# Optimization experiments

Measured on AMD Instinct MI355X. Metric: run time of the kernel, lower is better.

Reference implementation:

```python
import jax, jax.numpy as jnp
import numpy as np
import math

B, S, D_MODEL, H, D_LATENT = 2, 2048, 2048, 16, 512
D_HEAD = D_MODEL // H


def setup_inputs() -> dict:
    key = jax.random.key(0)
    ks = jax.random.split(key, 6)
    s = lambda fan: 1.0 / math.sqrt(fan)
    return {
        "x": jax.random.normal(ks[0], (B, S, D_MODEL), dtype=jnp.float32),
        "W_q": jax.random.normal(ks[1], (D_MODEL, D_MODEL), dtype=jnp.float32) * s(D_MODEL),
        "W_down_kv": jax.random.normal(ks[2], (D_LATENT, D_MODEL), dtype=jnp.float32) * s(D_MODEL),
        "W_up_k": jax.random.normal(ks[3], (H, D_HEAD, D_LATENT), dtype=jnp.float32) * s(D_LATENT),
        "W_up_v": jax.random.normal(ks[4], (H, D_HEAD, D_LATENT), dtype=jnp.float32) * s(D_LATENT),
        "W_o": jax.random.normal(ks[5], (D_MODEL, D_MODEL), dtype=jnp.float32) * s(D_MODEL),
    }


def reference(x, W_q, W_down_kv, W_up_k, W_up_v, W_o):
    b, s_len, d_model = x.shape
    # Q: (B, H, S, Dh)
    Q = (x @ W_q.T).reshape(b, s_len, H, D_HEAD).transpose(0, 2, 1, 3)
    # latent KV: (B, S, d_latent)
    C_kv = x @ W_down_kv.T
    # per-head up-projections fused into one einsum: (B, H, S, Dh)
    K = jnp.einsum("bsl,hdl->bhsd", C_kv, W_up_k)
    V = jnp.einsum("bsl,hdl->bhsd", C_kv, W_up_v)
    scores = jnp.einsum("bhsd,bhtd->bhst", Q, K) / math.sqrt(D_HEAD)
    attn = jax.nn.softmax(scores, axis=-1)  # dropout p=0 / eval -> identity
    out = jnp.einsum("bhst,bhtd->bhsd", attn, V)
    out = out.transpose(0, 2, 1, 3).reshape(b, s_len, H * D_HEAD)
    return out @ W_o.T
```

## Files before the change

kernel.cpp:

```cpp
#include <hip/hip_runtime.h>
#include <hip/hip_bf16.h>

typedef __hip_bfloat16 bf16;
typedef __attribute__((ext_vector_type(8))) short short8v;
typedef __attribute__((ext_vector_type(4))) short short4v;
typedef __attribute__((ext_vector_type(4))) float f32x4;
typedef __attribute__((ext_vector_type(16))) float f32x16;
typedef __attribute__((ext_vector_type(4))) unsigned int uint4v;
typedef unsigned int u32;

#define MFMA_16x16x32(a, b, c) __builtin_amdgcn_mfma_f32_16x16x32_bf16((a), (b), (c), 0, 0, 0)
#define MFMA_32x32x16(a, b, c) __builtin_amdgcn_mfma_f32_32x32x16_bf16((a), (b), (c), 0, 0, 0)

constexpr int Bc = 2, Sc = 2048, DMc = 2048, Hc = 16, DLc = 512, DHc = 128;

__device__ __forceinline__ void gload_lds16(const bf16* g, void* lds) {
  __builtin_amdgcn_global_load_lds(
      (const __attribute__((address_space(1))) void*)g,
      (__attribute__((address_space(3))) void*)lds, 16, 0, 0);
}

__device__ __forceinline__ unsigned short bf16bits(float f) {
  return __builtin_bit_cast(unsigned short, __float2bfloat16(f));
}

struct CvtArgs {
  const float* src[6];
  bf16* dst[6];
  unsigned int cum[6];
  unsigned int total4;
};

__global__ __launch_bounds__(256) void cvt_all_kernel(CvtArgs a)
{
  unsigned int i = blockIdx.x * 256 + threadIdx.x;
  const unsigned int stride = gridDim.x * 256;
  for (; i < a.total4; i += stride) {
    int s = 0;
#pragma unroll
    for (int k = 1; k < 6; ++k) s += (i >= a.cum[k]) ? 1 : 0;
    unsigned int off = (i - a.cum[s]) * 4;
    float4 v = *(const float4*)(a.src[s] + off);
    short4v p;
    p[0] = (short)bf16bits(v.x);
    p[1] = (short)bf16bits(v.y);
    p[2] = (short)bf16bits(v.z);
    p[3] = (short)bf16bits(v.w);
    *(short4v*)(a.dst[s] + off) = p;
  }
}

#define GPHASE(bufv, KK, MH)                                                \
  do {                                                                      \
    const char* ap_ = aR + (bufv) * 32768 + (KK) * 8192 + (MH) * 4096;      \
    const char* bp_ = bR + (bufv) * 32768 + (KK) * 8192;                    \
    short8v af_[4], bf_[4];                                                 \
    _Pragma("unroll")                                                       \
    for (int m4 = 0; m4 < 4; ++m4)                                          \
      af_[m4] = *(const short8v*)(ap_ + m4 * 1024);                         \
    _Pragma("unroll")                                                       \
    for (int n = 0; n < 4; ++n)                                             \
      bf_[n] = *(const short8v*)(bp_ + n * 1024);                           \
    __builtin_amdgcn_s_setprio(1);                                          \
    _Pragma("unroll")                                                       \
    for (int m4 = 0; m4 < 4; ++m4)                                          \
      _Pragma("unroll")                                                     \
      for (int n = 0; n < 4; ++n)                                           \
        acc[(MH) * 4 + m4][n] =                                             \
            MFMA_16x16x32(af_[m4], bf_[n], acc[(MH) * 4 + m4][n]);          \
    __builtin_amdgcn_s_setprio(0);                                          \
  } while (0)

template<int EPI>
__device__ __forceinline__ void gemm_tile_256(
    const bf16* __restrict__ A, const bf16* __restrict__ BT, void* __restrict__ Cv,
    int K, int ldc, int row0, int col0, char* AsC, char* BsC)
{
  const int tid = threadIdx.x;
  const int lane = tid & 63, wid = tid >> 6;
  const int wm = wid >> 2, wn = wid & 3;
  const int fr = lane & 15, g = lane >> 4;

  f32x4 acc[8][4] = {};

  const int srow = tid >> 2;
  const int scolS = ((tid & 3) * 16) ^ (((srow >> 1) & 3) << 4);
  const bf16* sA = A + (size_t)(row0 + srow) * K + (scolS >> 1);
  const bf16* sB = BT + (size_t)(col0 + srow) * K + (scolS >> 1);
  char* AsW = AsC + wid * 1024;
  char* BsW = BsC + wid * 1024;

  auto ISSA = [&](int buf, int h, int kk, int kt) {
    gload_lds16(sA + (size_t)(h * 128) * K + kt * 64 + kk * 32,
                AsW + buf * 32768 + h * 16384 + kk * 8192);
  };
  auto ISSB = [&](int buf, int h, int kk, int kt) {
    gload_lds16(sB + (size_t)(h * 128) * K + kt * 64 + kk * 32,
                BsW + buf * 32768 + h * 16384 + kk * 8192);
  };

  const int rdLane = fr * 64 + ((g * 16) ^ (((fr >> 1) & 3) << 4));
  const char* aR = AsC + wm * 16384 + rdLane;
  const char* bR = BsC + (wn >> 1) * 16384 + (wn & 1) * 4096 + rdLane;

  ISSA(0, 0, 0, 0); ISSA(0, 1, 0, 0); ISSB(0, 0, 0, 0); ISSB(0, 1, 0, 0);
  ISSA(0, 0, 1, 0); ISSA(0, 1, 1, 0); ISSB(0, 0, 1, 0); ISSB(0, 1, 1, 0);

  const int KT = K >> 6;
  for (int kt = 0; kt < KT - 1; ++kt) {
    const int buf = kt & 1, nb = buf ^ 1;
    asm volatile("s_waitcnt vmcnt(4)" ::: "memory");
    __builtin_amdgcn_s_barrier();
    asm volatile("" ::: "memory");
    ISSA(nb, 0, 0, kt + 1); ISSA(nb, 1, 0, kt + 1);
    GPHASE(buf, 0, 0);
    ISSB(nb, 0, 0, kt + 1); ISSB(nb, 1, 0, kt + 1);
    GPHASE(buf, 0, 1);
    asm volatile("s_waitcnt vmcnt(4)" ::: "memory");
    __builtin_amdgcn_s_barrier();
    asm volatile("" ::: "memory");
    ISSA(nb, 0, 1, kt + 1); ISSA(nb, 1, 1, kt + 1);
    GPHASE(buf, 1, 0);
    ISSB(nb, 0, 1, kt + 1); ISSB(nb, 1, 1, kt + 1);
    GPHASE(buf, 1, 1);
  }
  {
    const int buf = (KT - 1) & 1;
    asm volatile("s_waitcnt vmcnt(4)" ::: "memory");
    __builtin_amdgcn_s_barrier();
    asm volatile("" ::: "memory");
    GPHASE(buf, 0, 0);
    GPHASE(buf, 0, 1);
    asm volatile("s_waitcnt vmcnt(0)" ::: "memory");
    __builtin_amdgcn_s_barrier();
    asm volatile("" ::: "memory");
    GPHASE(buf, 1, 0);
    GPHASE(buf, 1, 1);
  }

  const int crow = g * 4, ccol = fr;
  if (EPI == 0) {
    bf16* C = (bf16*)Cv;
#pragma unroll
    for (int m = 0; m < 8; ++m)
#pragma unroll
      for (int n = 0; n < 4; ++n) {
        bf16* Cp = C + (size_t)(row0 + wm * 128 + m * 16 + crow) * ldc
                     + col0 + wn * 64 + n * 16 + ccol;
#pragma unroll
        for (int r = 0; r < 4; ++r)
          Cp[(size_t)r * ldc] = __float2bfloat16(acc[m][n][r]);
      }
  } else if (EPI == 1) {
    bf16* C = (bf16*)Cv;
#pragma unroll
    for (int m = 0; m < 8; ++m)
#pragma unroll
      for (int n = 0; n < 4; ++n) {
        short4v pk;
#pragma unroll
        for (int r = 0; r < 4; ++r)
          pk[r] = (short)bf16bits(acc[m][n][r]);
        bf16* Cp = C + (size_t)(col0 + wn * 64 + n * 16 + ccol) * ldc
                     + row0 + wm * 128 + m * 16 + crow;
        *(short4v*)Cp = pk;
      }
  } else {
    float* C = (float*)Cv;
#pragma unroll
    for (int m = 0; m < 8; ++m)
#pragma unroll
      for (int n = 0; n < 4; ++n) {
        float* Cp = C + (size_t)(row0 + wm * 128 + m * 16 + crow) * ldc
                      + col0 + wn * 64 + n * 16 + ccol;
#pragma unroll
        for (int r = 0; r < 4; ++r)
          Cp[(size_t)r * ldc] = acc[m][n][r];
      }
  }
}

__global__ __launch_bounds__(512, 2) void qkv_gemm_kernel(
    const bf16* __restrict__ xb, const bf16* __restrict__ Wqb,
    const bf16* __restrict__ Wdkvb, bf16* __restrict__ Qb, bf16* __restrict__ Ck)
{
  __shared__ char As[65536];
  __shared__ char Bs[65536];
  const int flat = blockIdx.x + 10 * blockIdx.y;
  const int role = (flat & 7) * 20 + (flat >> 3);
  const int bx = role % 10, by = role / 10;
  if (bx < 8)
    gemm_tile_256<0>(xb, Wqb, Qb, DMc, DMc, by * 256, bx * 256, As, Bs);
  else
    gemm_tile_256<0>(xb, Wdkvb, Ck, DMc, DLc, by * 256, (bx - 8) * 256, As, Bs);
}

__global__ __launch_bounds__(512, 2) void up_gemm_kernel(
    const bf16* __restrict__ Ck, const bf16* __restrict__ Wukb,
    const bf16* __restrict__ Wuvb, bf16* __restrict__ Kcat, bf16* __restrict__ VTcat)
{
  __shared__ char As[65536];
  __shared__ char Bs[65536];
  const int flat = blockIdx.x + 16 * blockIdx.y;
  const int role = (flat & 7) * 32 + (flat >> 3);
  const int bx = role & 15, by = role >> 4;
  if (bx < 8)
    gemm_tile_256<0>(Ck, Wukb, Kcat, DLc, DMc, by * 256, bx * 256, As, Bs);
  else
    gemm_tile_256<1>(Ck, Wuvb, VTcat, DLc, Bc * Sc, by * 256, (bx - 8) * 256, As, Bs);
}

__global__ __launch_bounds__(512, 2) void out_gemm_kernel(
    const bf16* __restrict__ AO, const bf16* __restrict__ Wob, float* __restrict__ out)
{
  __shared__ char As[65536];
  __shared__ char Bs[65536];
  const int flat = blockIdx.x + 8 * blockIdx.y;
  const int role = (flat & 7) * 16 + (flat >> 3);
  const int bx = role & 7, by = role >> 3;
  gemm_tile_256<2>(AO, Wob, out, DMc, DMc, by * 256, bx * 256, As, Bs);
}

constexpr int KVB = 64;
constexpr int NTT = Sc / KVB;
constexpr int VSTR = Bc * Sc;

__global__ __launch_bounds__(256, 2) void mla_attn_kernel(
    const bf16* __restrict__ Q, const bf16* __restrict__ Kcat,
    const bf16* __restrict__ VTcat, bf16* __restrict__ O)
{
  __shared__ bf16 Ks[2][KVB * 128];
  __shared__ bf16 Vs[2][64 * 128];

  const int tid = threadIdx.x, lane = tid & 63, wid = tid >> 6;
  const int l31 = lane & 31, hi = lane >> 5;

  const int flat = blockIdx.x + 16 * (blockIdx.y + 16 * blockIdx.z);
  const int role = (flat & 7) * 64 + (flat >> 3);
  const int qb = role & 15, h = (role >> 4) & 15, b = role >> 8;
  const int q0 = qb * 128 + wid * 32;

  const bf16* Qp = Q + (size_t)(b * Sc + q0 + l31) * DMc + h * DHc + hi * 8;
  short8v qf[8];
#pragma unroll
  for (int kk = 0; kk < 8; ++kk) qf[kk] = *(const short8v*)(Qp + kk * 16);

  const bf16* Kb = Kcat + (size_t)b * Sc * DMc + h * DHc;
  const bf16* Vb = VTcat + (size_t)(h * DHc) * VSTR + b * Sc;

  const int srow = wid * 4 + (lane >> 4);
  const int scolB = (lane & 15) * 16;
  const int swzK0 = ((srow & 7) << 4) ^ (((srow >> 3) & 1) << 6);
  const bf16* kpE = Kb + (size_t)srow * DMc + (((scolB ^ swzK0) & 255) >> 1);
  const bf16* kpO = Kb + (size_t)srow * DMc + ((((scolB ^ swzK0) ^ 128) & 255) >> 1);
  const int swzV0 = ((srow & 7) << 4) ^ (((srow >> 3) & 1) << 7);
  const int vcp = scolB ^ swzV0;
  const bf16* vp = Vb + (size_t)(2 * srow + (vcp >> 7)) * VSTR + ((vcp & 127) >> 1);

  auto STAGE = [&](int buf, int t0) {
    char* kd = (char*)(&Ks[buf][0]) + wid * 1024;
    gload_lds16(kpE + (size_t)t0 * DMc, kd);
    gload_lds16(kpO + (size_t)(t0 + 16) * DMc, kd + 4096);
    gload_lds16(kpE + (size_t)(t0 + 32) * DMc, kd + 8192);
    gload_lds16(kpO + (size_t)(t0 + 48) * DMc, kd + 12288);
    char* vd = (char*)(&Vs[buf][0]) + wid * 1024;
    const bf16* v0 = vp + t0;
    gload_lds16(v0, vd);
    gload_lds16(v0 + (size_t)32 * VSTR, vd + 4096);
    gload_lds16(v0 + (size_t)64 * VSTR, vd + 8192);
    gload_lds16(v0 + (size_t)96 * VSTR, vd + 12288);
  };

  const int swzR = ((l31 & 7) << 4) ^ (((l31 >> 3) & 1) << 6) ^ (((l31 >> 4) & 1) << 7);
  const int swzVR = (((l31 >> 1) & 7) << 4) ^ (((l31 >> 4) & 1) << 7);

  f32x16 oacc[4] = {};
  float m_r = -1e30f, l_r = 0.f, msc = 0.f;
  const float SCL2 = 0.12751650f;
  const float THRraw = 47.0f;

  STAGE(0, 0);
  int cur = 0;

  for (int it = 0; it < NTT; ++it) {
    asm volatile("s_waitcnt vmcnt(0)" ::: "memory");
    __builtin_amdgcn_s_barrier();
    asm volatile("" ::: "memory");
    if (it + 1 < NTT) STAGE(cur ^ 1, (it + 1) * KVB);
    asm volatile("" ::: "memory");

    f32x16 s0 = {}, s1 = {};
    const char* Kc = (const char*)(&Ks[cur][0]);
    __builtin_amdgcn_s_setprio(1);
#pragma unroll
    for (int kk = 0; kk < 8; ++kk) {
      const int cb = (kk * 32 + hi * 16) ^ swzR;
      short8v k0 = *(const short8v*)(Kc + l31 * 256 + cb);
      short8v k1 = *(const short8v*)(Kc + (32 + l31) * 256 + cb);
      s0 = MFMA_32x32x16(k0, qf[kk], s0);
      s1 = MFMA_32x32x16(k1, qf[kk], s1);
    }
    __builtin_amdgcn_s_setprio(0);

    float pm = s0[0];
#pragma unroll
    for (int i = 1; i < 16; ++i) pm = fmaxf(pm, s0[i]);
#pragma unroll
    for (int i = 0; i < 16; ++i) pm = fmaxf(pm, s1[i]);

    if (!__all(pm - m_r <= THRraw)) {
      float red = fmaxf(pm, __shfl_xor(pm, 32, 64));
      float mnew = fmaxf(m_r, red);
      float c = exp2f((m_r - mnew) * SCL2);
      m_r = mnew;
      msc = mnew * SCL2;
      l_r *= c;
#pragma unroll
      for (int db = 0; db < 4; ++db) oacc[db] *= c;
    }

    short8v pf[4];
#pragma unroll
    for (int tt = 0; tt < 2; ++tt) {
      const f32x16& s = tt ? s1 : s0;
#pragma unroll
      for (int half = 0; half < 2; ++half) {
        float e0 = exp2f(__builtin_fmaf(s[half * 8 + 0], SCL2, -msc));
        float e1 = exp2f(__builtin_fmaf(s[half * 8 + 1], SCL2, -msc));
        float e2 = exp2f(__builtin_fmaf(s[half * 8 + 2], SCL2, -msc));
        float e3 = exp2f(__builtin_fmaf(s[half * 8 + 3], SCL2, -msc));
        float e4 = exp2f(__builtin_fmaf(s[half * 8 + 4], SCL2, -msc));
        float e5 = exp2f(__builtin_fmaf(s[half * 8 + 5], SCL2, -msc));
        float e6 = exp2f(__builtin_fmaf(s[half * 8 + 6], SCL2, -msc));
        float e7 = exp2f(__builtin_fmaf(s[half * 8 + 7], SCL2, -msc));
        l_r += ((e0 + e1) + (e2 + e3)) + ((e4 + e5) + (e6 + e7));
        u32 cA, cB, cC, cD;
        asm("v_cvt_pk_bf16_f32 %0, %1, %2" : "=v"(cA) : "v"(e0), "v"(e1));
        asm("v_cvt_pk_bf16_f32 %0, %1, %2" : "=v"(cB) : "v"(e2), "v"(e3));
        asm("v_cvt_pk_bf16_f32 %0, %1, %2" : "=v"(cC) : "v"(e4), "v"(e5));
        asm("v_cvt_pk_bf16_f32 %0, %1, %2" : "=v"(cD) : "v"(e6), "v"(e7));
        asm volatile("v_permlane32_swap_b32 %0, %1" : "+v"(cA), "+v"(cC));
        asm volatile("v_permlane32_swap_b32 %0, %1" : "+v"(cB), "+v"(cD));
        uint4v w;
        w[0] = cA; w[1] = cB; w[2] = cC; w[3] = cD;
        pf[tt * 2 + half] = __builtin_bit_cast(short8v, w);
      }
    }

    const char* Vc = (const char*)(&Vs[cur][0]);
    __builtin_amdgcn_s_setprio(1);
#pragma unroll
    for (int db = 0; db < 4; ++db) {
      const int vrow = (db * 16 + (l31 >> 1)) * 256;
#pragma unroll
      for (int ts = 0; ts < 4; ++ts) {
        const int cb = ((l31 & 1) * 128 + ts * 32 + hi * 16) ^ swzVR;
        short8v vf = *(const short8v*)(Vc + vrow + cb);
        oacc[db] = MFMA_32x32x16(vf, pf[ts], oacc[db]);
      }
    }
    __builtin_amdgcn_s_setprio(0);

    cur ^= 1;
  }

  float l = l_r + __shfl_xor(l_r, 32, 64);
  float inv = 1.f / l;
  bf16* Op = O + (size_t)(b * Sc + q0 + l31) * DMc + h * DHc + hi * 4;
#pragma unroll
  for (int db = 0; db < 4; ++db) {
#pragma unroll
    for (int rq = 0; rq < 4; ++rq) {
      short4v pk;
#pragma unroll
      for (int r = 0; r < 4; ++r)
        pk[r] = (short)bf16bits(oacc[db][rq * 4 + r] * inv);
      *(short4v*)(Op + db * 32 + rq * 8) = pk;
    }
  }
}

extern "C" void kernel_launch(void* const* d_in, const int* in_sizes, int n_in,
                              void* d_out, int out_size, void* d_ws, size_t ws_size,
                              hipStream_t stream)
{
  const float* x    = (const float*)d_in[0];
  const float* Wq   = (const float*)d_in[1];
  const float* Wdkv = (const float*)d_in[2];
  const float* Wuk  = (const float*)d_in[3];
  const float* Wuv  = (const float*)d_in[4];
  const float* Wo   = (const float*)d_in[5];
  float* out = (float*)d_out;

  char* ws = (char*)d_ws;
  bf16* Qb    = (bf16*)(ws + 0);
  bf16* Kcat  = (bf16*)(ws + 16777216);
  bf16* VTcat = (bf16*)(ws + 33554432);
  bf16* xb    = (bf16*)(ws + 50331648);
  bf16* AO    = (bf16*)(ws + 50331648);
  bf16* Ck    = (bf16*)(ws + 67108864);
  bf16* Wqb   = (bf16*)(ws + 71303168);
  bf16* Wdkvb = (bf16*)(ws + 79691776);
  bf16* Wukb  = (bf16*)(ws + 81788928);
  bf16* Wuvb  = (bf16*)(ws + 83886080);
  bf16* Wob   = (bf16*)(ws + 85983232);

  dim3 blk(256, 1, 1);

  CvtArgs ca;
  ca.src[0] = x;    ca.dst[0] = xb;
  ca.src[1] = Wq;   ca.dst[1] = Wqb;
  ca.src[2] = Wdkv; ca.dst[2] = Wdkvb;
  ca.src[3] = Wuk;  ca.dst[3] = Wukb;
  ca.src[4] = Wuv;  ca.dst[4] = Wuvb;
  ca.src[5] = Wo;   ca.dst[5] = Wob;
  unsigned int n4[6] = { (unsigned)(Bc * Sc * DMc / 4), (unsigned)(DMc * DMc / 4),
                         (unsigned)(DLc * DMc / 4),     (unsigned)(Hc * DHc * DLc / 4),
                         (unsigned)(Hc * DHc * DLc / 4),(unsigned)(DMc * DMc / 4) };
  unsigned int acc = 0;
  for (int i = 0; i < 6; ++i) { ca.cum[i] = acc; acc += n4[i]; }
  ca.total4 = acc;
  cvt_all_kernel<<<2048, blk, 0, stream>>>(ca);

  qkv_gemm_kernel<<<dim3(10, 16), dim3(512, 1, 1), 0, stream>>>(xb, Wqb, Wdkvb, Qb, Ck);

  up_gemm_kernel<<<dim3(16, 16), dim3(512, 1, 1), 0, stream>>>(Ck, Wukb, Wuvb, Kcat, VTcat);

  mla_attn_kernel<<<dim3(Sc / 128, Hc, Bc), dim3(256, 1, 1), 0, stream>>>(
      Qb, Kcat, VTcat, AO);

  out_gemm_kernel<<<dim3(8, 16), dim3(512, 1, 1), 0, stream>>>(AO, Wob, out);
}
```

Before: 274.6 us.

## Replace 256-tile GEMMs for QKV and output projections with simple 128-tile kernel

Adds a simpler 128x128 GEMM tile that uses 256 threads, 16x16x32 MFMAs and a single-buffered 32-wide K loop. The QKV projection and output projection now use it in place of the pipelined 256x256 tile. This launches many more blocks (640 and 512 instead of 160 and 128) so the GPU's compute units are better filled. In exchange it gives up the double-buffered, software-pipelined loads and the larger per-block reuse of the 256 tile, and adds two barriers per K step.

```diff
diff --git a/kernel.cpp b/kernel.cpp
--- a/kernel.cpp
+++ b/kernel.cpp
@@ -48,6 +48,122 @@
     p[3] = (short)bf16bits(v.w);
     *(short4v*)(a.dst[s] + off) = p;
   }
+}
+
+template<int EPI>
+__device__ __forceinline__ void gemm_tile_128(
+    const bf16* __restrict__ A, const bf16* __restrict__ BT, void* __restrict__ Cv,
+    int K, int ldc, int row0, int col0, bf16* As, bf16* Bs)
+{
+  const int tid = threadIdx.x;
+  const int lane = tid & 63, wid = tid >> 6;
+  const int wr = wid >> 1, wc = wid & 1;
+
+  f32x4 acc[4][4] = {};
+
+  const int srow = tid >> 2;
+  const int scol = (tid & 3) * 8;
+  const bf16* Ag = A + (size_t)(row0 + srow) * K + scol;
+  const bf16* Bg = BT + (size_t)(col0 + srow) * K + scol;
+  char* AsW = (char*)As + wid * 1024;
+  char* BsW = (char*)Bs + wid * 1024;
+
+  const int fr = lane & 15, fk = (lane >> 4) * 8;
+  const bf16* aRd = As + (wr * 64 + fr) * 32 + fk;
+  const bf16* bRd = Bs + (wc * 64 + fr) * 32 + fk;
+
+  for (int k0 = 0; k0 < K; k0 += 32) {
+    gload_lds16(Ag, AsW);
+    gload_lds16(Ag + (size_t)64 * K, AsW + 4096);
+    gload_lds16(Bg, BsW);
+    gload_lds16(Bg + (size_t)64 * K, BsW + 4096);
+    Ag += 32; Bg += 32;
+    __syncthreads();
+    short8v a[4], b[4];
+#pragma unroll
+    for (int m = 0; m < 4; ++m) a[m] = *(const short8v*)(aRd + m * 16 * 32);
+#pragma unroll
+    for (int n = 0; n < 4; ++n) b[n] = *(const short8v*)(bRd + n * 16 * 32);
+#pragma unroll
+    for (int m = 0; m < 4; ++m)
+#pragma unroll
+      for (int n = 0; n < 4; ++n)
+        acc[m][n] = MFMA_16x16x32(a[m], b[n], acc[m][n]);
+    __syncthreads();
+  }
+
+  const int crow = (lane >> 4) * 4, ccol = lane & 15;
+  if (EPI == 0) {
+    bf16* C = (bf16*)Cv;
+#pragma unroll
+    for (int m = 0; m < 4; ++m)
+#pragma unroll
+      for (int n = 0; n < 4; ++n) {
+        bf16* Cp = C + (size_t)(row0 + wr * 64 + m * 16 + crow) * ldc
+                     + col0 + wc * 64 + n * 16 + ccol;
+#pragma unroll
+        for (int r = 0; r < 4; ++r)
+          Cp[(size_t)r * ldc] = __float2bfloat16(acc[m][n][r]);
+      }
+  } else if (EPI == 1) {
+    bf16* C = (bf16*)Cv;
+#pragma unroll
+    for (int m = 0; m < 4; ++m)
+#pragma unroll
+      for (int n = 0; n < 4; ++n) {
+        short4v pk;
+#pragma unroll
+        for (int r = 0; r < 4; ++r)
+          pk[r] = (short)bf16bits(acc[m][n][r]);
+        bf16* Cp = C + (size_t)(col0 + wc * 64 + n * 16 + ccol) * ldc
+                     + row0 + wr * 64 + m * 16 + crow;
+        *(short4v*)Cp = pk;
+      }
+  } else {
+    float* C = (float*)Cv;
+#pragma unroll
+    for (int m = 0; m < 4; ++m)
+#pragma unroll
+      for (int n = 0; n < 4; ++n) {
+        float* Cp = C + (size_t)(row0 + wr * 64 + m * 16 + crow) * ldc
+                      + col0 + wc * 64 + n * 16 + ccol;
+#pragma unroll
+        for (int r = 0; r < 4; ++r)
+          Cp[(size_t)r * ldc] = acc[m][n][r];
+      }
+  }
+}
+
+__device__ __forceinline__ int2 xcd_remap(int nx, int ny) {
+  int flat = blockIdx.x + nx * blockIdx.y;
+  int chunk = (nx * ny) >> 3;
+  int role = (flat & 7) * chunk + (flat >> 3);
+  return make_int2(role % nx, role / nx);
+}
+
+template<int EPI>
+__global__ __launch_bounds__(256) void gemm_bt_kernel(
+    const bf16* __restrict__ A, const bf16* __restrict__ BT, void* __restrict__ C,
+    int K, int N)
+{
+  __shared__ bf16 As[128 * 32];
+  __shared__ bf16 Bs[128 * 32];
+  int2 bb = xcd_remap(gridDim.x, gridDim.y);
+  gemm_tile_128<EPI>(A, BT, C, K, N, bb.y * 128, bb.x * 128, As, Bs);
+}
+
+__global__ __launch_bounds__(256) void qkv_gemm_kernel(
+    const bf16* __restrict__ xb, const bf16* __restrict__ Wqb,
+    const bf16* __restrict__ Wdkvb, bf16* __restrict__ Qb, bf16* __restrict__ Ck)
+{
+  __shared__ bf16 As[128 * 32];
+  __shared__ bf16 Bs[128 * 32];
+  int2 bb = xcd_remap(20, 32);
+  const int bx = bb.x, row0 = bb.y * 128;
+  if (bx < 16)
+    gemm_tile_128<0>(xb, Wqb, Qb, DMc, DMc, row0, bx * 128, As, Bs);
+  else
+    gemm_tile_128<0>(xb, Wdkvb, Ck, DMc, DLc, row0, (bx - 16) * 128, As, Bs);
 }
 
 #define GPHASE(bufv, KK, MH)                                                \
@@ -180,21 +296,6 @@
   }
 }
 
-__global__ __launch_bounds__(512, 2) void qkv_gemm_kernel(
-    const bf16* __restrict__ xb, const bf16* __restrict__ Wqb,
-    const bf16* __restrict__ Wdkvb, bf16* __restrict__ Qb, bf16* __restrict__ Ck)
-{
-  __shared__ char As[65536];
-  __shared__ char Bs[65536];
-  const int flat = blockIdx.x + 10 * blockIdx.y;
-  const int role = (flat & 7) * 20 + (flat >> 3);
-  const int bx = role % 10, by = role / 10;
-  if (bx < 8)
-    gemm_tile_256<0>(xb, Wqb, Qb, DMc, DMc, by * 256, bx * 256, As, Bs);
-  else
-    gemm_tile_256<0>(xb, Wdkvb, Ck, DMc, DLc, by * 256, (bx - 8) * 256, As, Bs);
-}
-
 __global__ __launch_bounds__(512, 2) void up_gemm_kernel(
     const bf16* __restrict__ Ck, const bf16* __restrict__ Wukb,
     const bf16* __restrict__ Wuvb, bf16* __restrict__ Kcat, bf16* __restrict__ VTcat)
@@ -208,17 +309,6 @@
     gemm_tile_256<0>(Ck, Wukb, Kcat, DLc, DMc, by * 256, bx * 256, As, Bs);
   else
     gemm_tile_256<1>(Ck, Wuvb, VTcat, DLc, Bc * Sc, by * 256, (bx - 8) * 256, As, Bs);
-}
-
-__global__ __launch_bounds__(512, 2) void out_gemm_kernel(
-    const bf16* __restrict__ AO, const bf16* __restrict__ Wob, float* __restrict__ out)
-{
-  __shared__ char As[65536];
-  __shared__ char Bs[65536];
-  const int flat = blockIdx.x + 8 * blockIdx.y;
-  const int role = (flat & 7) * 16 + (flat >> 3);
-  const int bx = role & 7, by = role >> 3;
-  gemm_tile_256<2>(AO, Wob, out, DMc, DMc, by * 256, bx * 256, As, Bs);
 }
 
 constexpr int KVB = 64;
@@ -422,12 +512,12 @@
   ca.total4 = acc;
   cvt_all_kernel<<<2048, blk, 0, stream>>>(ca);
 
-  qkv_gemm_kernel<<<dim3(10, 16), dim3(512, 1, 1), 0, stream>>>(xb, Wqb, Wdkvb, Qb, Ck);
+  qkv_gemm_kernel<<<dim3(20, 32), blk, 0, stream>>>(xb, Wqb, Wdkvb, Qb, Ck);
 
   up_gemm_kernel<<<dim3(16, 16), dim3(512, 1, 1), 0, stream>>>(Ck, Wukb, Wuvb, Kcat, VTcat);
 
   mla_attn_kernel<<<dim3(Sc / 128, Hc, Bc), dim3(256, 1, 1), 0, stream>>>(
       Qb, Kcat, VTcat, AO);
 
-  out_gemm_kernel<<<dim3(8, 16), dim3(512, 1, 1), 0, stream>>>(AO, Wob, out);
-}
+  gemm_bt_kernel<2><<<dim3(16, 32), blk, 0, stream>>>(AO, Wob, out, DMc, DMc);
+}
```

Result: faster. 235.5 us (median of 2 runs) (-14.2%).
